# Optimization experiments

Measured on AMD Instinct MI355X. Metric: run time of the kernel, lower is better.

Reference implementation:

```python
import jax, jax.numpy as jnp
import numpy as np

N = 8192
INPUT_DIM = 3000
HIDDEN_DIM = 512
LATENT_DIM = 30
AVG_DEGREE = 32


def setup_inputs() -> dict:
    key = jax.random.key(0)
    k_x, k_g, k_w0, k_v0, k_v1, k_w1 = jax.random.split(key, 6)

    node_features = jax.random.normal(k_x, (N, INPUT_DIM), dtype=jnp.float32)

    # Binary adjacency, avg degree ~AVG_DEGREE, with self-loops so every
    # softmax row has at least one entry (mirrors typical spatial graphs).
    p = AVG_DEGREE / N
    adj = (jax.random.uniform(k_g, (N, N)) < p).astype(jnp.float32)
    idx = jnp.arange(N)
    graph = adj.at[idx, idx].set(1.0)

    def xavier(k, shape):
        fan_in, fan_out = shape
        limit = float(np.sqrt(6.0 / (fan_in + fan_out)))
        return jax.random.uniform(k, shape, jnp.float32, -limit, limit)

    W0 = xavier(k_w0, (INPUT_DIM, HIDDEN_DIM))
    v0 = xavier(k_v0, (HIDDEN_DIM, 1))
    v1 = xavier(k_v1, (HIDDEN_DIM, 1))
    W1 = xavier(k_w1, (HIDDEN_DIM, LATENT_DIM))

    return {"node_features": node_features, "graph": graph,
            "W0": W0, "v0": v0, "v1": v1, "W1": W1}


def _gat_layer(X_in, graph, W, v0, v1):
    # Projection
    X = X_in @ W                                   # [N, D]
    # Rank-1 pairwise scores, masked by adjacency
    f0 = X @ v0                                    # [N, 1]
    f1 = X @ v1                                    # [N, 1]
    E = graph * (f0 + f1.T)                        # [N, N]
    scores = jax.nn.sigmoid(E) - 0.5               # values kept by to_sparse
    mask = graph != 0
    # Masked softmax over dim=1 (torch.sparse.softmax over nnz of each row;
    # rows with no edges stay all-zero after to_dense)
    neg = jnp.finfo(scores.dtype).min
    w = jnp.where(mask, scores, neg)
    m = jnp.max(w, axis=1, keepdims=True)
    e = jnp.where(mask, jnp.exp(w - m), 0.0)
    s = jnp.sum(e, axis=1, keepdims=True)
    alphas = e / jnp.maximum(s, jnp.asarray(1e-30, scores.dtype))
    # Weighted aggregation + ELU
    return jax.nn.elu(alphas @ X)


def reference(node_features, graph, W0, v0, v1, W1):
    Z = _gat_layer(node_features, graph, W0, v0, v1)  # layer 0 (attention)
    Z = Z @ W1                                        # last layer: proj only
    return Z
```

## Files before the change

### kernel.cpp

```cpp
#include <hip/hip_runtime.h>
#include <stdint.h>

#define NN   8192
#define KDIM 3000
#define KP   3072
#define DDIM 512
#define LDIM 30

typedef __attribute__((ext_vector_type(8))) short short8;
typedef __attribute__((ext_vector_type(4))) float float4v;

__device__ __forceinline__ float bf2f(unsigned short h) {
    union { unsigned int u; float f; } v; v.u = ((unsigned int)h) << 16; return v.f;
}
__device__ __forceinline__ unsigned short f2bf(float f) {
    union { float f; unsigned int u; } v; v.f = f;
    unsigned int r = v.u + 0x7FFF + ((v.u >> 16) & 1);
    return (unsigned short)(r >> 16);
}
__device__ __forceinline__ void gl_lds16(const void* g, void* l) {
    __builtin_amdgcn_global_load_lds(
        (const __attribute__((address_space(1))) unsigned int*)g,
        (__attribute__((address_space(3))) unsigned int*)l, 16, 0, 0);
}

__global__ __launch_bounds__(384) void k_convertA(
    const float* __restrict__ A, unsigned short* __restrict__ Abf) {
    int row = blockIdx.x, t = threadIdx.x;
    int k = t * 8;
    uint4 o = {0, 0, 0, 0};
    if (k < KDIM) {
        const float* src = A + (size_t)row * KDIM + k;
        float4 a = *(const float4*)src;
        float4 b = *(const float4*)(src + 4);
        unsigned short* h = (unsigned short*)&o;
        h[0] = f2bf(a.x); h[1] = f2bf(a.y); h[2] = f2bf(a.z); h[3] = f2bf(a.w);
        h[4] = f2bf(b.x); h[5] = f2bf(b.y); h[6] = f2bf(b.z); h[7] = f2bf(b.w);
    }
    *(uint4*)(Abf + (size_t)row * KP + k) = o;
}

__global__ void k_prepW(const float* __restrict__ W0,
                        unsigned short* __restrict__ W0T) {
    __shared__ float tile[32][33];
    int t = threadIdx.x;
    int tx = t & 31, ty = t >> 5;
    int k0 = blockIdx.x * 32, n0 = blockIdx.y * 32;
    #pragma unroll
    for (int p = 0; p < 4; p++) {
        int k = k0 + ty + p * 8;
        float val = 0.f;
        if (k < KDIM) val = W0[(size_t)k * DDIM + n0 + tx];
        tile[ty + p * 8][tx] = val;
    }
    __syncthreads();
    #pragma unroll
    for (int p = 0; p < 4; p++) {
        int k = k0 + tx;
        int n = n0 + ty + p * 8;
        W0T[(size_t)n * KP + k] = f2bf(tile[tx][ty + p * 8]);
    }
}

#define BM 128
#define BN 64

__global__ __launch_bounds__(256) void k_gemm(
    const unsigned short* __restrict__ A,
    const unsigned short* __restrict__ BT,
    float* __restrict__ X,
    unsigned short* __restrict__ Xbf)
{
    __shared__ __align__(16) unsigned short As[2][BM][32];
    __shared__ __align__(16) unsigned short Bs[2][BN][32];
    int t = threadIdx.x, w = t >> 6, l = t & 63;
    int m0 = blockIdx.x * BM, n0 = blockIdx.y * BN;
    int wm = (w & 1) * 64, wn = (w >> 1) * 32;

    float4v acc[4][2];
    #pragma unroll
    for (int mf = 0; mf < 4; mf++)
        #pragma unroll
        for (int nf = 0; nf < 2; nf++)
            acc[mf][nf] = (float4v){0.f, 0.f, 0.f, 0.f};

    int lr = l >> 2;
    int lk = (l & 3) * 8;
    const unsigned short* Abase = A  + (size_t)m0 * KP;
    const unsigned short* Bbase = BT + (size_t)n0 * KP;
    const int lA = l & 15;
    const int qA = (l >> 4) * 8;

    for (int k0 = 0; k0 < KP; k0 += 64) {
        if (k0) __syncthreads();
        #pragma unroll
        for (int p = 0; p < 4; p++) {
            int q = w * 4 + p, h = q >> 3, rb = q & 7;
            gl_lds16(Abase + (size_t)(rb * 16 + lr) * KP + k0 + h * 32 + lk,
                     &As[h][rb * 16][0]);
        }
        #pragma unroll
        for (int p = 0; p < 2; p++) {
            int q = w * 2 + p, h = q >> 2, rb = q & 3;
            gl_lds16(Bbase + (size_t)(rb * 16 + lr) * KP + k0 + h * 32 + lk,
                     &Bs[h][rb * 16][0]);
        }
        __syncthreads();

        #pragma unroll
        for (int h = 0; h < 2; h++) {
            short8 af[4], bfr[2];
            #pragma unroll
            for (int mf = 0; mf < 4; mf++)
                af[mf] = *(const short8*)&As[h][wm + mf * 16 + lA][qA];
            #pragma unroll
            for (int nf = 0; nf < 2; nf++)
                bfr[nf] = *(const short8*)&Bs[h][wn + nf * 16 + lA][qA];
            #pragma unroll
            for (int mf = 0; mf < 4; mf++)
                #pragma unroll
                for (int nf = 0; nf < 2; nf++)
                    acc[mf][nf] = __builtin_amdgcn_mfma_f32_16x16x32_bf16(
                        af[mf], bfr[nf], acc[mf][nf], 0, 0, 0);
        }
    }

    int rq = (l >> 4) * 4;
    #pragma unroll
    for (int mf = 0; mf < 4; mf++) {
        #pragma unroll
        for (int nf = 0; nf < 2; nf++) {
            int col = n0 + wn + nf * 16 + lA;
            int row = m0 + wm + mf * 16 + rq;
            #pragma unroll
            for (int r = 0; r < 4; r++) {
                float v = acc[mf][nf][r];
                X  [(size_t)(row + r) * DDIM + col] = v;
                Xbf[(size_t)(row + r) * DDIM + col] = f2bf(v);
            }
        }
    }
}

__global__ __launch_bounds__(256) void k_f01(
    const float* __restrict__ X,
    const float* __restrict__ v0,
    const float* __restrict__ v1,
    float* __restrict__ f0, float* __restrict__ f1)
{
    int w = threadIdx.x >> 6, l = threadIdx.x & 63;
    int i = blockIdx.x * 4 + w;
    const float* xr = X + (size_t)i * DDIM + l * 8;
    float4 xa = *(const float4*)(xr);
    float4 xb = *(const float4*)(xr + 4);
    float4 a0 = *(const float4*)(v0 + l * 8);
    float4 b0 = *(const float4*)(v0 + l * 8 + 4);
    float4 a1 = *(const float4*)(v1 + l * 8);
    float4 b1 = *(const float4*)(v1 + l * 8 + 4);
    float p0 = xa.x*a0.x + xa.y*a0.y + xa.z*a0.z + xa.w*a0.w
             + xb.x*b0.x + xb.y*b0.y + xb.z*b0.z + xb.w*b0.w;
    float p1 = xa.x*a1.x + xa.y*a1.y + xa.z*a1.z + xa.w*a1.w
             + xb.x*b1.x + xb.y*b1.y + xb.z*b1.z + xb.w*b1.w;
    #pragma unroll
    for (int off = 32; off; off >>= 1) {
        p0 += __shfl_down(p0, off);
        p1 += __shfl_down(p1, off);
    }
    if (l == 0) { f0[i] = p0; f1[i] = p1; }
}

#define CAP 1024
__global__ __launch_bounds__(256) void k_aggregate(
    const float* __restrict__ G,
    const unsigned short* __restrict__ Xbf,
    const float* __restrict__ f0,
    const float* __restrict__ f1,
    const float* __restrict__ W1,
    float* __restrict__ out)
{
    __shared__ int cnt;
    __shared__ int   jlist[CAP];
    __shared__ float elist[CAP];
    __shared__ float zrow[DDIM];
    __shared__ float red[256];
    int t = threadIdx.x;
    int i = blockIdx.x;
    if (t == 0) cnt = 0;
    __syncthreads();

    float f0i = f0[i];
    const float* grow = G + (size_t)i * NN;
    #pragma unroll
    for (int it = 0; it < 8; it++) {
        int base = (it * 256 + t) * 4;
        float4 gv = *(const float4*)(grow + base);
        float g[4] = {gv.x, gv.y, gv.z, gv.w};
        #pragma unroll
        for (int m = 0; m < 4; m++) {
            if (g[m] != 0.f) {
                int j = base + m;
                float xe = f0i + f1[j];
                float sg = 1.0f / (1.0f + __expf(-xe));
                float e  = __expf(sg - 0.5f);
                int p = atomicAdd(&cnt, 1);
                if (p < CAP) { jlist[p] = j; elist[p] = e; }
            }
        }
    }
    __syncthreads();

    int n = cnt < CAP ? cnt : CAP;
    float s = 0.f;
    for (int k = 0; k < n; k++) s += elist[k];
    float inv = 1.0f / fmaxf(s, 1e-30f);

    float a0 = 0.f, a1 = 0.f;
    int k = 0;
    for (; k + 4 <= n; k += 4) {
        int j0 = jlist[k], j1 = jlist[k+1], j2 = jlist[k+2], j3 = jlist[k+3];
        float e0 = elist[k], e1 = elist[k+1], e2 = elist[k+2], e3 = elist[k+3];
        unsigned int x0 = *(const unsigned int*)(Xbf + (size_t)j0 * DDIM + t * 2);
        unsigned int x1 = *(const unsigned int*)(Xbf + (size_t)j1 * DDIM + t * 2);
        unsigned int x2 = *(const unsigned int*)(Xbf + (size_t)j2 * DDIM + t * 2);
        unsigned int x3 = *(const unsigned int*)(Xbf + (size_t)j3 * DDIM + t * 2);
        a0 += e0 * bf2f((unsigned short)(x0 & 0xFFFFu))
            + e1 * bf2f((unsigned short)(x1 & 0xFFFFu))
            + e2 * bf2f((unsigned short)(x2 & 0xFFFFu))
            + e3 * bf2f((unsigned short)(x3 & 0xFFFFu));
        a1 += e0 * bf2f((unsigned short)(x0 >> 16))
            + e1 * bf2f((unsigned short)(x1 >> 16))
            + e2 * bf2f((unsigned short)(x2 >> 16))
            + e3 * bf2f((unsigned short)(x3 >> 16));
    }
    for (; k < n; k++) {
        int j = jlist[k];
        float e = elist[k];
        unsigned int xw = *(const unsigned int*)(Xbf + (size_t)j * DDIM + t * 2);
        a0 += e * bf2f((unsigned short)(xw & 0xFFFFu));
        a1 += e * bf2f((unsigned short)(xw >> 16));
    }
    a0 *= inv; a1 *= inv;
    zrow[2 * t]     = a0 > 0.f ? a0 : __expf(a0) - 1.0f;
    zrow[2 * t + 1] = a1 > 0.f ? a1 : __expf(a1) - 1.0f;
    __syncthreads();

    int c = t & 31, slab = t >> 5;
    float p = 0.f;
    if (c < LDIM) {
        #pragma unroll 4
        for (int q = 0; q < 64; q++) {
            int d = slab * 64 + q;
            p += zrow[d] * W1[d * LDIM + c];
        }
    }
    red[t] = p;
    __syncthreads();
    if (t < LDIM) {
        float sum = 0.f;
        #pragma unroll
        for (int s2 = 0; s2 < 8; s2++) sum += red[s2 * 32 + t];
        out[(size_t)i * LDIM + t] = sum;
    }
}

extern "C" void kernel_launch(void* const* d_in, const int* in_sizes, int n_in,
                              void* d_out, int out_size, void* d_ws, size_t ws_size,
                              hipStream_t stream) {
    (void)in_sizes; (void)n_in; (void)out_size; (void)ws_size;
    const float* nf = (const float*)d_in[0];
    const float* G  = (const float*)d_in[1];
    const float* W0 = (const float*)d_in[2];
    const float* v0 = (const float*)d_in[3];
    const float* v1 = (const float*)d_in[4];
    const float* W1 = (const float*)d_in[5];
    float* out = (float*)d_out;

    char* ws = (char*)d_ws;
    unsigned short* Abf = (unsigned short*)(ws);
    unsigned short* W0T = (unsigned short*)(ws + 50331648);
    float*          X   = (float*)(ws + 50331648 + 3145728);
    unsigned short* Xbf = (unsigned short*)(ws + 50331648 + 3145728 + 16777216);
    float* f0 = (float*)(ws + 50331648 + 3145728 + 16777216 + 8388608);
    float* f1 = (float*)(ws + 50331648 + 3145728 + 16777216 + 8388608 + 32768);

    hipLaunchKernelGGL(k_convertA, dim3(8192), dim3(384), 0, stream, nf, Abf);
    hipLaunchKernelGGL(k_prepW, dim3(96, 16), dim3(256), 0, stream, W0, W0T);
    hipLaunchKernelGGL(k_gemm, dim3(64, 8), dim3(256), 0, stream, Abf, W0T, X, Xbf);
    hipLaunchKernelGGL(k_f01, dim3(2048), dim3(256), 0, stream, X, v0, v1, f0, f1);
    hipLaunchKernelGGL(k_aggregate, dim3(8192), dim3(256), 0, stream, G, Xbf, f0, f1, W1, out);
}
```

Before: 516.8 us.

## Split-K the projection GEMM and fuse prep and combine kernels

Splits the bf16 projection GEMM into two K halves (grid z=2), which doubles the block count from 512 to 1024 to improve CU occupancy on the 256-CU device. A new combine kernel sums the two fp32 partials, writes the bf16 X, and computes f0/f1 in one pass. It also merges the A conversion and W0 transpose into one launch. The cost is an extra 16 MB fp32 partial write and read, and the larger workspace footprint.

```diff
diff --git a/kernel.cpp b/kernel.cpp
--- a/kernel.cpp
+++ b/kernel.cpp
@@ -4,6 +4,7 @@
 #define NN   8192
 #define KDIM 3000
 #define KP   3072
+#define KHALF 1536
 #define DDIM 512
 #define LDIM 30
 
@@ -24,41 +25,45 @@
         (__attribute__((address_space(3))) unsigned int*)l, 16, 0, 0);
 }
 
-__global__ __launch_bounds__(384) void k_convertA(
-    const float* __restrict__ A, unsigned short* __restrict__ Abf) {
-    int row = blockIdx.x, t = threadIdx.x;
-    int k = t * 8;
-    uint4 o = {0, 0, 0, 0};
-    if (k < KDIM) {
-        const float* src = A + (size_t)row * KDIM + k;
-        float4 a = *(const float4*)src;
-        float4 b = *(const float4*)(src + 4);
-        unsigned short* h = (unsigned short*)&o;
-        h[0] = f2bf(a.x); h[1] = f2bf(a.y); h[2] = f2bf(a.z); h[3] = f2bf(a.w);
-        h[4] = f2bf(b.x); h[5] = f2bf(b.y); h[6] = f2bf(b.z); h[7] = f2bf(b.w);
-    }
-    *(uint4*)(Abf + (size_t)row * KP + k) = o;
-}
-
-__global__ void k_prepW(const float* __restrict__ W0,
-                        unsigned short* __restrict__ W0T) {
-    __shared__ float tile[32][33];
-    int t = threadIdx.x;
-    int tx = t & 31, ty = t >> 5;
-    int k0 = blockIdx.x * 32, n0 = blockIdx.y * 32;
-    #pragma unroll
-    for (int p = 0; p < 4; p++) {
-        int k = k0 + ty + p * 8;
-        float val = 0.f;
-        if (k < KDIM) val = W0[(size_t)k * DDIM + n0 + tx];
-        tile[ty + p * 8][tx] = val;
-    }
-    __syncthreads();
-    #pragma unroll
-    for (int p = 0; p < 4; p++) {
-        int k = k0 + tx;
-        int n = n0 + ty + p * 8;
-        W0T[(size_t)n * KP + k] = f2bf(tile[tx][ty + p * 8]);
+__global__ __launch_bounds__(384) void k_prep(
+    const float* __restrict__ A, unsigned short* __restrict__ Abf,
+    const float* __restrict__ W0, unsigned short* __restrict__ W0T) {
+    int bid = blockIdx.x, t = threadIdx.x;
+    if (bid < NN) {
+        int k = t * 8;
+        uint4 o = {0, 0, 0, 0};
+        if (k < KDIM) {
+            const float* src = A + (size_t)bid * KDIM + k;
+            float4 a = *(const float4*)src;
+            float4 b = *(const float4*)(src + 4);
+            unsigned short* h = (unsigned short*)&o;
+            h[0] = f2bf(a.x); h[1] = f2bf(a.y); h[2] = f2bf(a.z); h[3] = f2bf(a.w);
+            h[4] = f2bf(b.x); h[5] = f2bf(b.y); h[6] = f2bf(b.z); h[7] = f2bf(b.w);
+        }
+        *(uint4*)(Abf + (size_t)bid * KP + k) = o;
+    } else {
+        __shared__ float tile[32][33];
+        int b = bid - NN;
+        int k0 = (b % 96) * 32, n0 = (b / 96) * 32;
+        int tx = t & 31, ty = (t >> 5) & 7;
+        if (t < 256) {
+            #pragma unroll
+            for (int p = 0; p < 4; p++) {
+                int k = k0 + ty + p * 8;
+                float val = 0.f;
+                if (k < KDIM) val = W0[(size_t)k * DDIM + n0 + tx];
+                tile[ty + p * 8][tx] = val;
+            }
+        }
+        __syncthreads();
+        if (t < 256) {
+            #pragma unroll
+            for (int p = 0; p < 4; p++) {
+                int k = k0 + tx;
+                int n = n0 + ty + p * 8;
+                W0T[(size_t)n * KP + k] = f2bf(tile[tx][ty + p * 8]);
+            }
+        }
     }
 }
 
@@ -68,13 +73,13 @@
 __global__ __launch_bounds__(256) void k_gemm(
     const unsigned short* __restrict__ A,
     const unsigned short* __restrict__ BT,
-    float* __restrict__ X,
-    unsigned short* __restrict__ Xbf)
+    float* __restrict__ Xpart)
 {
     __shared__ __align__(16) unsigned short As[2][BM][32];
     __shared__ __align__(16) unsigned short Bs[2][BN][32];
     int t = threadIdx.x, w = t >> 6, l = t & 63;
     int m0 = blockIdx.x * BM, n0 = blockIdx.y * BN;
+    int z  = blockIdx.z;
     int wm = (w & 1) * 64, wn = (w >> 1) * 32;
 
     float4v acc[4][2];
@@ -90,9 +95,10 @@
     const unsigned short* Bbase = BT + (size_t)n0 * KP;
     const int lA = l & 15;
     const int qA = (l >> 4) * 8;
-
-    for (int k0 = 0; k0 < KP; k0 += 64) {
-        if (k0) __syncthreads();
+    const int kstart = z * KHALF, kend = kstart + KHALF;
+
+    for (int k0 = kstart; k0 < kend; k0 += 64) {
+        if (k0 != kstart) __syncthreads();
         #pragma unroll
         for (int p = 0; p < 4; p++) {
             int q = w * 4 + p, h = q >> 3, rb = q & 7;
@@ -125,6 +131,7 @@
         }
     }
 
+    float* Xp = Xpart + (size_t)z * NN * DDIM;
     int rq = (l >> 4) * 4;
     #pragma unroll
     for (int mf = 0; mf < 4; mf++) {
@@ -133,40 +140,39 @@
             int col = n0 + wn + nf * 16 + lA;
             int row = m0 + wm + mf * 16 + rq;
             #pragma unroll
-            for (int r = 0; r < 4; r++) {
-                float v = acc[mf][nf][r];
-                X  [(size_t)(row + r) * DDIM + col] = v;
-                Xbf[(size_t)(row + r) * DDIM + col] = f2bf(v);
-            }
-        }
-    }
-}
-
-__global__ __launch_bounds__(256) void k_f01(
-    const float* __restrict__ X,
-    const float* __restrict__ v0,
-    const float* __restrict__ v1,
-    float* __restrict__ f0, float* __restrict__ f1)
+            for (int r = 0; r < 4; r++)
+                Xp[(size_t)(row + r) * DDIM + col] = acc[mf][nf][r];
+        }
+    }
+}
+
+__global__ __launch_bounds__(256) void k_combine(
+    const float* __restrict__ X0, const float* __restrict__ X1,
+    const float* __restrict__ v0, const float* __restrict__ v1,
+    unsigned short* __restrict__ Xbf, float* __restrict__ f0, float* __restrict__ f1)
 {
-    int w = threadIdx.x >> 6, l = threadIdx.x & 63;
-    int i = blockIdx.x * 4 + w;
-    const float* xr = X + (size_t)i * DDIM + l * 8;
-    float4 xa = *(const float4*)(xr);
-    float4 xb = *(const float4*)(xr + 4);
-    float4 a0 = *(const float4*)(v0 + l * 8);
-    float4 b0 = *(const float4*)(v0 + l * 8 + 4);
-    float4 a1 = *(const float4*)(v1 + l * 8);
-    float4 b1 = *(const float4*)(v1 + l * 8 + 4);
-    float p0 = xa.x*a0.x + xa.y*a0.y + xa.z*a0.z + xa.w*a0.w
-             + xb.x*b0.x + xb.y*b0.y + xb.z*b0.z + xb.w*b0.w;
-    float p1 = xa.x*a1.x + xa.y*a1.y + xa.z*a1.z + xa.w*a1.w
-             + xb.x*b1.x + xb.y*b1.y + xb.z*b1.z + xb.w*b1.w;
+    __shared__ float r0[4], r1[4];
+    int i = blockIdx.x, t = threadIdx.x;
+    int w = t >> 6, l = t & 63;
+    size_t base = (size_t)i * DDIM + t * 2;
+    float2 xa = *(const float2*)(X0 + base);
+    float2 xb = *(const float2*)(X1 + base);
+    float x0 = xa.x + xb.x, x1 = xa.y + xb.y;
+    unsigned int pack = (unsigned int)f2bf(x0) | ((unsigned int)f2bf(x1) << 16);
+    *(unsigned int*)(Xbf + base) = pack;
+    float2 va = *(const float2*)(v0 + t * 2);
+    float2 vb = *(const float2*)(v1 + t * 2);
+    float p0 = x0 * va.x + x1 * va.y;
+    float p1 = x0 * vb.x + x1 * vb.y;
     #pragma unroll
     for (int off = 32; off; off >>= 1) {
         p0 += __shfl_down(p0, off);
         p1 += __shfl_down(p1, off);
     }
-    if (l == 0) { f0[i] = p0; f1[i] = p1; }
+    if (l == 0) { r0[w] = p0; r1[w] = p1; }
+    __syncthreads();
+    if (t == 0) f0[i] = r0[0] + r0[1] + r0[2] + r0[3];
+    if (t == 1) f1[i] = r1[0] + r1[1] + r1[2] + r1[3];
 }
 
 #define CAP 1024
@@ -276,16 +282,17 @@
     float* out = (float*)d_out;
 
     char* ws = (char*)d_ws;
-    unsigned short* Abf = (unsigned short*)(ws);
-    unsigned short* W0T = (unsigned short*)(ws + 50331648);
-    float*          X   = (float*)(ws + 50331648 + 3145728);
-    unsigned short* Xbf = (unsigned short*)(ws + 50331648 + 3145728 + 16777216);
-    float* f0 = (float*)(ws + 50331648 + 3145728 + 16777216 + 8388608);
-    float* f1 = (float*)(ws + 50331648 + 3145728 + 16777216 + 8388608 + 32768);
-
-    hipLaunchKernelGGL(k_convertA, dim3(8192), dim3(384), 0, stream, nf, Abf);
-    hipLaunchKernelGGL(k_prepW, dim3(96, 16), dim3(256), 0, stream, W0, W0T);
-    hipLaunchKernelGGL(k_gemm, dim3(64, 8), dim3(256), 0, stream, Abf, W0T, X, Xbf);
-    hipLaunchKernelGGL(k_f01, dim3(2048), dim3(256), 0, stream, X, v0, v1, f0, f1);
-    hipLaunchKernelGGL(k_aggregate, dim3(8192), dim3(256), 0, stream, G, Xbf, f0, f1, W1, out);
-}
+    size_t off = 0;
+    unsigned short* Abf = (unsigned short*)(ws + off); off += (size_t)NN * KP * 2;
+    unsigned short* W0T = (unsigned short*)(ws + off); off += (size_t)DDIM * KP * 2;
+    float*          Xp  = (float*)(ws + off);          off += (size_t)2 * NN * DDIM * 4;
+    unsigned short* Xbf = (unsigned short*)(ws + off); off += (size_t)NN * DDIM * 2;
+    float* f0 = (float*)(ws + off); off += NN * 4;
+    float* f1 = (float*)(ws + off); off += NN * 4;
+
+    hipLaunchKernelGGL(k_prep, dim3(NN + 1536), dim3(384), 0, stream, nf, Abf, W0, W0T);
+    hipLaunchKernelGGL(k_gemm, dim3(64, 8, 2), dim3(256), 0, stream, Abf, W0T, Xp);
+    hipLaunchKernelGGL(k_combine, dim3(NN), dim3(256), 0, stream,
+                       Xp, Xp + (size_t)NN * DDIM, v0, v1, Xbf, f0, f1);
+    hipLaunchKernelGGL(k_aggregate, dim3(NN), dim3(256), 0, stream, G, Xbf, f0, f1, W1, out);
+}
```

Result: no change. 512.3 us (-0.9%).
